# Kernel tuning notes

Hardware: AMD Instinct MI355X
Metric: run time of the kernel (lower is better)

Reference implementation:

```python
import jax, jax.numpy as jnp
import numpy as np

K, D = 512, 64


def setup_inputs() -> dict:
    key = jax.random.key(0)
    k1, k2 = jax.random.split(key)
    z_e_x = jax.random.normal(k1, (32, 4096, D), dtype=jnp.float32)
    # nn.Embedding weight initialized uniform(-1/K, 1/K)
    codebook = jax.random.uniform(k2, (K, D), dtype=jnp.float32,
                                  minval=-1.0 / K, maxval=1.0 / K)
    return {"z_e_x": z_e_x, "codebook": codebook}


def reference(z_e_x, codebook):
    # vq(): pairwise squared L2 distances to codebook, then argmin.
    d = z_e_x.shape[-1]
    flat = z_e_x.reshape(-1, d)                                   # [N, D]
    # ||z||^2 - 2 z.e + ||e||^2  (addmm form from original vq)
    dists = (jnp.sum(flat * flat, axis=1, keepdims=True)
             - 2.0 * flat @ codebook.T
             + jnp.sum(codebook * codebook, axis=1))              # [N, K]
    indices = jnp.argmin(dists, axis=1)                            # [N]
    # latents: indices reshaped to input shape minus feature dim
    return indices.reshape(z_e_x.shape[:-1])
```

## Files before the change

### kernel.cpp

```cpp
#include <hip/hip_runtime.h>
#include <math.h>

#define K_CODES 512
#define D_DIM   64
#define BM      512
#define THREADS 512
#define LSTR    72
#define CLS     65
#define EPS_GAP 6e-5f

#define WS_CNT_OFF  2048
#define WS_EH_OFF   4096
#define WS_EL_OFF   77824
#define WS_LIST_OFF 151552

typedef __attribute__((ext_vector_type(8))) short short8v;
typedef __attribute__((ext_vector_type(4))) float f32x4;

__device__ __forceinline__ float np_sumsq64(const float* zarr) {
    float L[16];
#pragma unroll
    for (int j = 0; j < 16; ++j)
        L[j] = __fadd_rn(
            __fadd_rn(__fmul_rn(zarr[j],      zarr[j]),
                      __fmul_rn(zarr[j + 16], zarr[j + 16])),
            __fadd_rn(__fmul_rn(zarr[j + 32], zarr[j + 32]),
                      __fmul_rn(zarr[j + 48], zarr[j + 48])));
    float m[8];
#pragma unroll
    for (int j = 0; j < 8; ++j) m[j] = __fadd_rn(L[j], L[j + 8]);
    float n4[4];
#pragma unroll
    for (int j = 0; j < 4; ++j) n4[j] = __fadd_rn(m[j], m[j + 4]);
    return __fadd_rn(__fadd_rn(n4[0], n4[2]), __fadd_rn(n4[1], n4[3]));
}

__device__ __forceinline__ unsigned short f32_bf16_rne(float x) {
    unsigned int u = __float_as_uint(x);
    unsigned int r = (u + 0x7FFFu + ((u >> 16) & 1u)) >> 16;
    return (unsigned short)r;
}
__device__ __forceinline__ float bf16_f32(unsigned short h) {
    return __uint_as_float(((unsigned int)h) << 16);
}
__device__ __forceinline__ void split2(float x, unsigned short& h, unsigned short& l) {
    h = f32_bf16_rne(x);
    l = f32_bf16_rne(x - bf16_f32(h));
}

__global__ __launch_bounds__(256)
void vq_prep_kernel(const float* __restrict__ cb, float* __restrict__ ws,
                    int do_split) {
    int g = blockIdx.x * blockDim.x + threadIdx.x;
    if (g == 0) *reinterpret_cast<int*>((char*)ws + WS_CNT_OFF) = 0;
    int k = g >> 2, q = g & 3;
    if (k >= K_CODES) return;
    const float* row = cb + (size_t)k * D_DIM;
    if (q == 0) {
        float e[D_DIM];
        const float4* p = reinterpret_cast<const float4*>(row);
#pragma unroll
        for (int i = 0; i < 16; ++i) {
            float4 v = p[i];
            e[4*i+0]=v.x; e[4*i+1]=v.y; e[4*i+2]=v.z; e[4*i+3]=v.w;
        }
        ws[k] = np_sumsq64(e);
    }
    if (do_split) {
        unsigned short* eh = reinterpret_cast<unsigned short*>((char*)ws + WS_EH_OFF)
                             + (size_t)k * LSTR;
        unsigned short* el = reinterpret_cast<unsigned short*>((char*)ws + WS_EL_OFF)
                             + (size_t)k * LSTR;
#pragma unroll
        for (int i = 16 * q; i < 16 * q + 16; ++i) {
            unsigned short h, l;
            split2(row[i], h, l);
            eh[i] = h; el[i] = l;
        }
        if (q == 3)
#pragma unroll
            for (int i = D_DIM; i < LSTR; ++i) { eh[i] = 0; el[i] = 0; }
    }
}

__global__ __launch_bounds__(512)
void vq_pass1_mono(const float* __restrict__ z,
                   const unsigned short* __restrict__ eh_g,
                   const unsigned short* __restrict__ el_g,
                   const float* __restrict__ norms, int* __restrict__ out,
                   int* __restrict__ cnt, int* __restrict__ list, int cap, int n) {
    __shared__ __align__(16) unsigned short ehS[K_CODES * LSTR];
    __shared__ __align__(16) unsigned short elS[K_CODES * LSTR];
    __shared__ __align__(16) float nrmS[K_CODES];

    const int tid  = threadIdx.x;
    const int l    = tid & 63;
    const int w    = tid >> 6;
    const int j    = l >> 4;
    const int c16  = l & 15;
    const int j4   = j * 4;
    const int base = blockIdx.x * BM;

    {
        const char* esrc = (const char*)eh_g;
        const char* lsrc = (const char*)el_g;
#pragma unroll
        for (int r = 0; r < 9; ++r) {
            size_t off = ((size_t)tid + (size_t)r * THREADS) * 16;
            __builtin_amdgcn_global_load_lds(
                (const __attribute__((address_space(1))) void*)(esrc + off),
                (__attribute__((address_space(3))) void*)((char*)ehS + off), 16, 0, 0);
            __builtin_amdgcn_global_load_lds(
                (const __attribute__((address_space(1))) void*)(lsrc + off),
                (__attribute__((address_space(3))) void*)((char*)elS + off), 16, 0, 0);
        }
        if (tid < K_CODES / 4)
            reinterpret_cast<float4*>(nrmS)[tid] =
                reinterpret_cast<const float4*>(norms)[tid];
    }

    short8v bzh[4][2], bzl[4][2];
#pragma unroll
    for (int p = 0; p < 4; ++p) {
        int row = base + (4 * w + p) * 16 + c16;
        if (row >= n) row = n - 1;
        const float* zp = z + (size_t)row * D_DIM + j * 8;
#pragma unroll
        for (int h = 0; h < 2; ++h) {
            float4 v0 = *reinterpret_cast<const float4*>(zp + h * 32);
            float4 v1 = *reinterpret_cast<const float4*>(zp + h * 32 + 4);
            unsigned short hh[8], ll[8];
            split2(-2.0f * v0.x, hh[0], ll[0]); split2(-2.0f * v0.y, hh[1], ll[1]);
            split2(-2.0f * v0.z, hh[2], ll[2]); split2(-2.0f * v0.w, hh[3], ll[3]);
            split2(-2.0f * v1.x, hh[4], ll[4]); split2(-2.0f * v1.y, hh[5], ll[5]);
            split2(-2.0f * v1.z, hh[6], ll[6]); split2(-2.0f * v1.w, hh[7], ll[7]);
            short8v th, tl;
#pragma unroll
            for (int i = 0; i < 8; ++i) { th[i] = (short)hh[i]; tl[i] = (short)ll[i]; }
            bzh[p][h] = th; bzl[p][h] = tl;
        }
    }

    __syncthreads();

    float m1[4] = {INFINITY, INFINITY, INFINITY, INFINITY};
    float m2[4] = {INFINITY, INFINITY, INFINITY, INFINITY};

#pragma unroll 4
    for (int cti = 0; cti < 32; ++cti) {
        const int ct = (cti + 4 * w) & 31;
        int ar = (ct * 16 + c16) * LSTR + j * 8;
        short8v aeh0 = *reinterpret_cast<const short8v*>(&ehS[ar]);
        short8v aeh1 = *reinterpret_cast<const short8v*>(&ehS[ar + 32]);
        short8v ael0 = *reinterpret_cast<const short8v*>(&elS[ar]);
        short8v ael1 = *reinterpret_cast<const short8v*>(&elS[ar + 32]);
        float4 nr = *reinterpret_cast<const float4*>(&nrmS[ct * 16 + j4]);
        f32x4 nrv = {nr.x, nr.y, nr.z, nr.w};

        f32x4 acc[4];
#pragma unroll
        for (int p = 0; p < 4; ++p) acc[p] = nrv;
        __builtin_amdgcn_s_setprio(1);
#pragma unroll
        for (int p = 0; p < 4; ++p) {
            acc[p] = __builtin_amdgcn_mfma_f32_16x16x32_bf16(aeh0, bzh[p][0], acc[p], 0, 0, 0);
            acc[p] = __builtin_amdgcn_mfma_f32_16x16x32_bf16(aeh1, bzh[p][1], acc[p], 0, 0, 0);
            acc[p] = __builtin_amdgcn_mfma_f32_16x16x32_bf16(aeh0, bzl[p][0], acc[p], 0, 0, 0);
            acc[p] = __builtin_amdgcn_mfma_f32_16x16x32_bf16(aeh1, bzl[p][1], acc[p], 0, 0, 0);
            acc[p] = __builtin_amdgcn_mfma_f32_16x16x32_bf16(ael0, bzh[p][0], acc[p], 0, 0, 0);
            acc[p] = __builtin_amdgcn_mfma_f32_16x16x32_bf16(ael1, bzh[p][1], acc[p], 0, 0, 0);
        }
        __builtin_amdgcn_s_setprio(0);

        const unsigned kb = (unsigned)(ct * 16) | (unsigned)j4;
#pragma unroll
        for (int p = 0; p < 4; ++p) {
#pragma unroll
            for (int r = 0; r < 4; ++r) {
                unsigned bits = (__float_as_uint(acc[p][r]) & 0xFFFFFE00u)
                                | (kb + (unsigned)r);
                float pk = __uint_as_float(bits);
                m2[p] = fminf(m2[p], fmaxf(m1[p], pk));
                m1[p] = fminf(m1[p], pk);
            }
        }
    }

#pragma unroll
    for (int p = 0; p < 4; ++p) {
        float a1 = m1[p], a2 = m2[p];
#pragma unroll
        for (int off = 16; off <= 32; off <<= 1) {
            float o1 = __shfl_xor(a1, off, 64);
            float o2 = __shfl_xor(a2, off, 64);
            a2 = fminf(fminf(a2, o2), fmaxf(a1, o1));
            a1 = fminf(a1, o1);
        }
        int  ptg    = base + (4 * w + p) * 16 + c16;
        bool writer = (j == 0) && (ptg < n);
        bool flag   = writer && (a2 - a1 <= EPS_GAP);
        unsigned long long m = __ballot(flag);
        int abase = 0;
        if (m) {
            int leader = __ffsll(m) - 1;
            if (l == leader) abase = atomicAdd(cnt, __popcll(m));
            abase = __shfl(abase, leader, 64);
        }
        if (writer) {
            int val = (int)(__float_as_uint(a1) & 0x1FFu);
            if (flag) {
                int rank = __popcll(m & ((1ull << l) - 1ull));
                int slot = abase + rank;
                if (slot < cap) list[slot] = ptg;
                else            val |= (int)0x80000000;
            }
            out[ptg] = val;
        }
    }
}

__global__ __launch_bounds__(256)
void vq_pass1_legacy(const float* __restrict__ z, const float* __restrict__ cb,
                     const float* __restrict__ norms, int* __restrict__ out,
                     int* __restrict__ cnt, int* __restrict__ list, int cap, int n) {
    __shared__ unsigned short zhS[128 * LSTR];
    __shared__ unsigned short zlS[128 * LSTR];
    __shared__ unsigned short ehS[128 * LSTR];
    __shared__ unsigned short elS[128 * LSTR];
    __shared__ float nrmL[128];

    const int tid  = threadIdx.x;
    const int l    = tid & 63;
    const int w    = tid >> 6;
    const int j    = l >> 4;
    const int c16  = l & 15;
    const int base = blockIdx.x * 128;

    const float4* z4 = reinterpret_cast<const float4*>(z);
#pragma unroll
    for (int rep = 0; rep < 8; ++rep) {
        int flat = rep * 256 + tid;
        int pt   = flat >> 4;
        int dblk = flat & 15;
        int gp = base + pt; if (gp >= n) gp = n - 1;
        float4 v = z4[(size_t)gp * 16 + dblk];
        ushort4 h, lo;
        split2(v.x, h.x, lo.x); split2(v.y, h.y, lo.y);
        split2(v.z, h.z, lo.z); split2(v.w, h.w, lo.w);
        *reinterpret_cast<ushort4*>(&zhS[pt * LSTR + dblk * 4]) = h;
        *reinterpret_cast<ushort4*>(&zlS[pt * LSTR + dblk * 4]) = lo;
    }
    __syncthreads();

    short8v bzh[2][2], bzl[2][2];
#pragma unroll
    for (int p = 0; p < 2; ++p) {
        int pr = ((2 * w + p) * 16 + c16) * LSTR;
#pragma unroll
        for (int h = 0; h < 2; ++h) {
            int off = pr + h * 32 + j * 8;
            bzh[p][h] = *reinterpret_cast<const short8v*>(&zhS[off]);
            bzl[p][h] = *reinterpret_cast<const short8v*>(&zlS[off]);
        }
    }

    float m1[2] = {INFINITY, INFINITY};
    float m2[2] = {INFINITY, INFINITY};
    int   i1[2] = {0, 0};

    for (int c = 0; c < 4; ++c) {
        __syncthreads();
        const float4* cb4 = reinterpret_cast<const float4*>(cb);
#pragma unroll
        for (int rep = 0; rep < 8; ++rep) {
            int flat = rep * 256 + tid;
            int code = flat >> 4;
            int dblk = flat & 15;
            float4 v = cb4[(size_t)(c * 128 + code) * 16 + dblk];
            ushort4 h, lo;
            split2(v.x, h.x, lo.x); split2(v.y, h.y, lo.y);
            split2(v.z, h.z, lo.z); split2(v.w, h.w, lo.w);
            *reinterpret_cast<ushort4*>(&ehS[code * LSTR + dblk * 4]) = h;
            *reinterpret_cast<ushort4*>(&elS[code * LSTR + dblk * 4]) = lo;
        }
        if (tid < 32)
            reinterpret_cast<float4*>(nrmL)[tid] =
                reinterpret_cast<const float4*>(norms)[c * 32 + tid];
        __syncthreads();

#pragma unroll
        for (int ct = 0; ct < 8; ++ct) {
            int ar = (ct * 16 + c16) * LSTR + j * 8;
            short8v aeh0 = *reinterpret_cast<const short8v*>(&ehS[ar]);
            short8v aeh1 = *reinterpret_cast<const short8v*>(&ehS[ar + 32]);
            short8v ael0 = *reinterpret_cast<const short8v*>(&elS[ar]);
            short8v ael1 = *reinterpret_cast<const short8v*>(&elS[ar + 32]);
            float4 nr = *reinterpret_cast<const float4*>(&nrmL[ct * 16 + j * 4]);
            float nra[4] = {nr.x, nr.y, nr.z, nr.w};
            int kg0 = c * 128 + ct * 16 + j * 4;
#pragma unroll
            for (int p = 0; p < 2; ++p) {
                f32x4 acc = {0.f, 0.f, 0.f, 0.f};
                acc = __builtin_amdgcn_mfma_f32_16x16x32_bf16(aeh0, bzh[p][0], acc, 0, 0, 0);
                acc = __builtin_amdgcn_mfma_f32_16x16x32_bf16(aeh1, bzh[p][1], acc, 0, 0, 0);
                acc = __builtin_amdgcn_mfma_f32_16x16x32_bf16(aeh0, bzl[p][0], acc, 0, 0, 0);
                acc = __builtin_amdgcn_mfma_f32_16x16x32_bf16(aeh1, bzl[p][1], acc, 0, 0, 0);
                acc = __builtin_amdgcn_mfma_f32_16x16x32_bf16(ael0, bzh[p][0], acc, 0, 0, 0);
                acc = __builtin_amdgcn_mfma_f32_16x16x32_bf16(ael1, bzh[p][1], acc, 0, 0, 0);
#pragma unroll
                for (int r = 0; r < 4; ++r) {
                    float s = fmaf(-2.0f, acc[r], nra[r]);
                    int kg = kg0 + r;
                    bool lt1 = s < m1[p];
                    float nm2 = lt1 ? m1[p] : fminf(s, m2[p]);
                    i1[p] = lt1 ? kg : i1[p];
                    m1[p] = lt1 ? s : m1[p];
                    m2[p] = nm2;
                }
            }
        }
    }

#pragma unroll
    for (int p = 0; p < 2; ++p) {
        float a1 = m1[p], a2 = m2[p]; int ai = i1[p];
#pragma unroll
        for (int off = 16; off <= 32; off <<= 1) {
            float o1 = __shfl_xor(a1, off, 64);
            float o2 = __shfl_xor(a2, off, 64);
            int   oi = __shfl_xor(ai, off, 64);
            float hi = fmaxf(a1, o1);
            bool take = o1 < a1;
            ai = take ? oi : ai;
            a1 = take ? o1 : a1;
            a2 = fminf(hi, fminf(a2, o2));
        }
        int  ptg    = base + (2 * w + p) * 16 + c16;
        bool writer = (j == 0) && (ptg < n);
        bool flag   = writer && (a2 - a1 <= EPS_GAP);
        unsigned long long m = __ballot(flag);
        int abase = 0;
        if (m) {
            int leader = __ffsll(m) - 1;
            if (l == leader) abase = atomicAdd(cnt, __popcll(m));
            abase = __shfl(abase, leader, 64);
        }
        if (writer) {
            int val = ai;
            if (flag) {
                int rank = __popcll(m & ((1ull << l) - 1ull));
                int slot = abase + rank;
                if (slot < cap) list[slot] = ptg;
                else            val |= (int)0x80000000;
            }
            out[ptg] = val;
        }
    }
}

__global__ __launch_bounds__(256)
void vq_cleanup_kernel(const float* __restrict__ z, const float* __restrict__ cb,
                       const float* __restrict__ norms,
                       const int* __restrict__ cnt, const int* __restrict__ list,
                       int cap, int* __restrict__ out, int n) {
    __shared__ float cbS[K_CODES * CLS];
    __shared__ float rbv[4];
    __shared__ int   rbi[4];
    const int tid  = threadIdx.x;
    const int lane = tid & 63;
    const int wv   = tid >> 6;

    {
        const float4* cb4 = reinterpret_cast<const float4*>(cb);
        for (int i = tid; i < K_CODES * 16; i += 256) {
            float4 v = cb4[i];
            int row = i >> 4, col = (i & 15) * 4;
            float* d = &cbS[row * CLS + col];
            d[0] = v.x; d[1] = v.y; d[2] = v.z; d[3] = v.w;
        }
    }
    __syncthreads();

    int total = *cnt;
    int lim   = total < cap ? total : cap;

    for (int i = blockIdx.x; i < lim; i += gridDim.x) {
        int pt = list[i];
        float zr[D_DIM];
        const float4* zp = reinterpret_cast<const float4*>(z + (size_t)pt * D_DIM);
#pragma unroll
        for (int g = 0; g < 16; ++g) {
            float4 q = zp[g];
            zr[4*g+0]=q.x; zr[4*g+1]=q.y; zr[4*g+2]=q.z; zr[4*g+3]=q.w;
        }
        const float sz = np_sumsq64(zr);
        float best = INFINITY; int bi = 0x7FFFFFFF;
#pragma unroll 1
        for (int rr = 0; rr < 2; ++rr) {
            int k = tid + rr * 256;
            const float* e = &cbS[k * CLS];
            float a = 0.f;
#pragma unroll
            for (int d = 0; d < D_DIM; ++d)
                a = fmaf(zr[d], e[d], a);
            float s = __fadd_rn(__fsub_rn(sz, __fmul_rn(2.0f, a)), norms[k]);
            if (s < best || (s == best && k < bi)) { best = s; bi = k; }
        }
#pragma unroll
        for (int off = 1; off < 64; off <<= 1) {
            float os = __shfl_xor(best, off, 64);
            int   ok = __shfl_xor(bi, off, 64);
            if (os < best || (os == best && ok < bi)) { best = os; bi = ok; }
        }
        if (lane == 0) { rbv[wv] = best; rbi[wv] = bi; }
        __syncthreads();
        if (tid == 0) {
            float b = rbv[0]; int id = rbi[0];
#pragma unroll
            for (int q = 1; q < 4; ++q) {
                float v = rbv[q]; int vi = rbi[q];
                if (v < b || (v == b && vi < id)) { b = v; id = vi; }
            }
            out[pt] = id;
        }
        __syncthreads();
    }

    if (total > cap) {
        const int wid    = (blockIdx.x * blockDim.x + tid) >> 6;
        const int nwaves = (gridDim.x * blockDim.x) >> 6;
        for (int b = wid * 64; b < n; b += nwaves * 64) {
            int t = b + lane;
            int v = (t < n) ? out[t] : 0;
            unsigned long long m = __ballot(v < 0);
            while (m) {
                int bb = __ffsll(m) - 1;
                m &= m - 1ull;
                int pt = b + bb;
                float zr[D_DIM];
                const float4* zp = reinterpret_cast<const float4*>(z + (size_t)pt * D_DIM);
#pragma unroll
                for (int g = 0; g < 16; ++g) {
                    float4 q = zp[g];
                    zr[4*g+0]=q.x; zr[4*g+1]=q.y; zr[4*g+2]=q.z; zr[4*g+3]=q.w;
                }
                const float sz = np_sumsq64(zr);
                float best = INFINITY; int bi = 0x7FFFFFFF;
#pragma unroll 1
                for (int r = 0; r < 8; ++r) {
                    int k = lane * 8 + r;
                    const float* e = &cbS[k * CLS];
                    float a = 0.f;
#pragma unroll
                    for (int d = 0; d < D_DIM; ++d)
                        a = fmaf(zr[d], e[d], a);
                    float s = __fadd_rn(__fsub_rn(sz, __fmul_rn(2.0f, a)), norms[k]);
                    if (s < best) { best = s; bi = k; }
                }
#pragma unroll
                for (int off = 1; off < 64; off <<= 1) {
                    float os = __shfl_xor(best, off, 64);
                    int   ok = __shfl_xor(bi, off, 64);
                    if (os < best || (os == best && ok < bi)) { best = os; bi = ok; }
                }
                if (lane == 0) out[pt] = bi;
            }
        }
    }
}

extern "C" void kernel_launch(void* const* d_in, const int* in_sizes, int n_in,
                              void* d_out, int out_size, void* d_ws, size_t ws_size,
                              hipStream_t stream) {
    const float* z  = (const float*)d_in[0];
    const float* cb = (const float*)d_in[1];
    int n = in_sizes[0] / D_DIM;
    float* norms = (float*)d_ws;
    int*   cnt   = (int*)((char*)d_ws + WS_CNT_OFF);
    int* out = (int*)d_out;

    bool fast = ws_size >= (size_t)WS_LIST_OFF + 4096;
    vq_prep_kernel<<<(4 * K_CODES + 255) / 256, 256, 0, stream>>>(cb, norms, fast ? 1 : 0);

    if (fast) {
        const unsigned short* eh = (const unsigned short*)((char*)d_ws + WS_EH_OFF);
        const unsigned short* el = (const unsigned short*)((char*)d_ws + WS_EL_OFF);
        int* list = (int*)((char*)d_ws + WS_LIST_OFF);
        int  cap  = (int)((ws_size - WS_LIST_OFF) / 4);
        vq_pass1_mono<<<(n + BM - 1) / BM, THREADS, 0, stream>>>(
            z, eh, el, norms, out, cnt, list, cap, n);
        vq_cleanup_kernel<<<256, 256, 0, stream>>>(z, cb, norms, cnt, list, cap, out, n);
    } else {
        int* list = (int*)d_ws + 513;
        int  cap  = (int)(ws_size / 4) - 513; if (cap < 0) cap = 0;
        vq_pass1_legacy<<<(n + 127) / 128, 256, 0, stream>>>(
            z, cb, norms, out, cnt, list, cap, n);
        vq_cleanup_kernel<<<256, 256, 0, stream>>>(z, cb, norms, cnt, list, cap, out, n);
    }
}
```

Measured before the change: 63.77 us.

## Drop shared-memory codebook staging in cleanup kernel, read codebook from global

The cleanup kernel no longer copies the whole 512x64 codebook (about 133KB with padding) into shared memory per block. Instead each thread reads its codebook rows directly from global memory as float4 and relies on the cache. The grid grows from 256 to 2048 blocks, and the fallback tolerance EPS_GAP is tightened so fewer points get flagged for exact recomputation. This removes a large per-block staging cost and the occupancy limit of a huge LDS footprint. The trade-off is more global and L2 traffic per point, and a risk of mis-flagging near-ties at the tighter gap.

Result: no change. 63.22 us (-0.9%).

```diff
diff --git a/kernel.cpp b/kernel.cpp
--- a/kernel.cpp
+++ b/kernel.cpp
@@ -6,8 +6,7 @@
 #define BM      512
 #define THREADS 512
 #define LSTR    72
-#define CLS     65
-#define EPS_GAP 6e-5f
+#define EPS_GAP 4.5e-5f
 
 #define WS_CNT_OFF  2048
 #define WS_EH_OFF   4096
@@ -363,24 +362,12 @@
                        const float* __restrict__ norms,
                        const int* __restrict__ cnt, const int* __restrict__ list,
                        int cap, int* __restrict__ out, int n) {
-    __shared__ float cbS[K_CODES * CLS];
     __shared__ float rbv[4];
     __shared__ int   rbi[4];
     const int tid  = threadIdx.x;
     const int lane = tid & 63;
     const int wv   = tid >> 6;
 
-    {
-        const float4* cb4 = reinterpret_cast<const float4*>(cb);
-        for (int i = tid; i < K_CODES * 16; i += 256) {
-            float4 v = cb4[i];
-            int row = i >> 4, col = (i & 15) * 4;
-            float* d = &cbS[row * CLS + col];
-            d[0] = v.x; d[1] = v.y; d[2] = v.z; d[3] = v.w;
-        }
-    }
-    __syncthreads();
-
     int total = *cnt;
     int lim   = total < cap ? total : cap;
 
@@ -396,13 +383,18 @@
         const float sz = np_sumsq64(zr);
         float best = INFINITY; int bi = 0x7FFFFFFF;
 #pragma unroll 1
-        for (int rr = 0; rr < 2; ++rr) {
-            int k = tid + rr * 256;
-            const float* e = &cbS[k * CLS];
+        for (int r = 0; r < 2; ++r) {
+            int k = tid * 2 + r;
+            const float4* e4 = reinterpret_cast<const float4*>(cb) + ((size_t)k << 4);
             float a = 0.f;
 #pragma unroll
-            for (int d = 0; d < D_DIM; ++d)
-                a = fmaf(zr[d], e[d], a);
+            for (int g = 0; g < 16; ++g) {
+                float4 q = e4[g];
+                a = fmaf(zr[4*g+0], q.x, a);
+                a = fmaf(zr[4*g+1], q.y, a);
+                a = fmaf(zr[4*g+2], q.z, a);
+                a = fmaf(zr[4*g+3], q.w, a);
+            }
             float s = __fadd_rn(__fsub_rn(sz, __fmul_rn(2.0f, a)), norms[k]);
             if (s < best || (s == best && k < bi)) { best = s; bi = k; }
         }
@@ -448,14 +440,20 @@
                 float best = INFINITY; int bi = 0x7FFFFFFF;
 #pragma unroll 1
                 for (int r = 0; r < 8; ++r) {
-                    int k = lane * 8 + r;
-                    const float* e = &cbS[k * CLS];
+                    const float4* e4 = reinterpret_cast<const float4*>(cb) +
+                                       ((size_t)(lane * 8 + r) << 4);
                     float a = 0.f;
 #pragma unroll
-                    for (int d = 0; d < D_DIM; ++d)
-                        a = fmaf(zr[d], e[d], a);
-                    float s = __fadd_rn(__fsub_rn(sz, __fmul_rn(2.0f, a)), norms[k]);
-                    if (s < best) { best = s; bi = k; }
+                    for (int g = 0; g < 16; ++g) {
+                        float4 q = e4[g];
+                        a = fmaf(zr[4*g+0], q.x, a);
+                        a = fmaf(zr[4*g+1], q.y, a);
+                        a = fmaf(zr[4*g+2], q.z, a);
+                        a = fmaf(zr[4*g+3], q.w, a);
+                    }
+                    float s = __fadd_rn(__fsub_rn(sz, __fmul_rn(2.0f, a)),
+                                        norms[lane * 8 + r]);
+                    if (s < best) { best = s; bi = lane * 8 + r; }
                 }
 #pragma unroll
                 for (int off = 1; off < 64; off <<= 1) {
@@ -489,12 +487,12 @@
         int  cap  = (int)((ws_size - WS_LIST_OFF) / 4);
         vq_pass1_mono<<<(n + BM - 1) / BM, THREADS, 0, stream>>>(
             z, eh, el, norms, out, cnt, list, cap, n);
-        vq_cleanup_kernel<<<256, 256, 0, stream>>>(z, cb, norms, cnt, list, cap, out, n);
+        vq_cleanup_kernel<<<2048, 256, 0, stream>>>(z, cb, norms, cnt, list, cap, out, n);
     } else {
         int* list = (int*)d_ws + 513;
         int  cap  = (int)(ws_size / 4) - 513; if (cap < 0) cap = 0;
         vq_pass1_legacy<<<(n + 127) / 128, 256, 0, stream>>>(
             z, cb, norms, out, cnt, list, cap, n);
-        vq_cleanup_kernel<<<256, 256, 0, stream>>>(z, cb, norms, cnt, list, cap, out, n);
-    }
-}
+        vq_cleanup_kernel<<<2048, 256, 0, stream>>>(z, cb, norms, cnt, list, cap, out, n);
+    }
+}
```
